# Kernel tuning notes

Hardware: AMD Instinct MI355X
Metric: run time of the kernel (lower is better)

## Reference

```python
import jax, jax.numpy as jnp
import numpy as np

LMAX = 3
D_IRREP = (LMAX + 1) ** 2  # 16
EPS = 1e-5


def _conv1d(x, w, pad):
    # x: [N, C_in, L], w: [C_out, C_in, K] -> [N, C_out, L]
    return jax.lax.conv_general_dilated(
        x, w, window_strides=(1,), padding=[(pad, pad)],
        dimension_numbers=("NCH", "OIH", "NCH"))


def setup_inputs() -> dict:
    key = jax.random.key(0)
    ks = jax.random.split(key, 8)
    B, Cin, Cout, N, K, RES = 128, 256, 256, 64, 5, 8
    return {
        "x": jax.random.normal(ks[0], (B, Cin * D_IRREP, N), jnp.float32),
        "weight": jax.random.normal(ks[1], (LMAX + 1, Cout, Cin, K), jnp.float32) / np.sqrt(Cin * K).astype(np.float32),
        "bias": jax.random.normal(ks[2], (1, 1, Cout), jnp.float32) * 0.02,
        "affine_weight": jnp.ones((LMAX + 1, Cout), jnp.float32),
        "gating_w": jax.random.normal(ks[3], (Cout, Cout), jnp.float32) / np.sqrt(Cout).astype(np.float32),
        "gating_b": jnp.zeros((Cout,), jnp.float32),
        "to_grid": jax.random.normal(ks[4], (RES, RES, D_IRREP), jnp.float32) * 0.3,
        "from_grid": jax.random.normal(ks[5], (RES, RES, D_IRREP), jnp.float32) * 0.3,
    }


def reference(x, weight, bias, affine_weight, gating_w, gating_b, to_grid, from_grid):
    B, CI, N = x.shape
    Cin = CI // D_IRREP
    Cout = weight.shape[1]
    pad = weight.shape[-1] // 2
    x = x.reshape(B, Cin, D_IRREP, N)

    # per-degree Conv1d over the time axis, irrep order folded into batch
    h_parts = []
    for l in range(LMAX + 1):
        lo, li = l * l, 2 * l + 1
        x_l = x[:, :, lo:lo + li, :]                                  # [B, Cin, li, N]
        x_l = x_l.transpose(0, 2, 1, 3).reshape(B * li, Cin, N)       # (b i) c n
        h_l = _conv1d(x_l, weight[l], pad)                            # [B*li, Cout, N]
        h_l = h_l.reshape(B, li, Cout, N).transpose(0, 3, 1, 2).reshape(B * N, li, Cout)  # (b n) i c
        if l == 0:
            h_l = h_l + bias
        h_parts.append(h_l)
    h = jnp.concatenate(h_parts, axis=1)                              # [B*N, 16, Cout]

    # rms_norm_sh: center l=0 over channels, degree-balanced RMS, per-degree affine
    degrees = np.repeat(np.arange(LMAX + 1), 2 * np.arange(LMAX + 1) + 1)  # [16]
    bal = jnp.asarray((1.0 / (2.0 * degrees + 1.0)) / (LMAX + 1), h.dtype)  # [16]
    mean0 = jnp.mean(h[:, :1, :], axis=2, keepdims=True)
    h = jnp.concatenate([h[:, :1, :] - mean0, h[:, 1:, :]], axis=1)
    var = jnp.einsum("zic,i->zc", h * h, bal)                         # [Z, C]
    inv = jax.lax.rsqrt(jnp.mean(var, axis=-1)[:, None, None] + EPS)  # [Z,1,1]
    h = h * inv * affine_weight[degrees][None]                        # [Z,16,C]

    # SeparableS2Activation: SiLU-gated scalars + S2 grid activation for l>0
    gate = jax.nn.silu(h[:, :1, :] @ gating_w.T + gating_b)           # [Z,1,C]
    grid = jax.nn.silu(jnp.einsum("bai,zic->zbac", to_grid, h))       # [Z,8,8,C]
    s2 = jnp.einsum("bai,zbac->zic", from_grid, grid)                 # [Z,16,C]
    h = jnp.concatenate([gate, s2[:, 1:, :]], axis=1)

    # (b n) i c -> b (c i) n
    out = h.reshape(B, N, D_IRREP, Cout).transpose(0, 3, 2, 1).reshape(B, Cout * D_IRREP, N)
    return out
```

## Files before the change

kernel.cpp:

```cpp
#include <hip/hip_runtime.h>
#include <hip/hip_bf16.h>

#define BB    128
#define CIN   256
#define COUT  256
#define NN    64
#define KW    5
#define DIRR  16
#define ZTOT  (BB*NN)
#define SX    264

typedef __attribute__((ext_vector_type(4))) float f32x4;
typedef __attribute__((ext_vector_type(8))) short s16x8;

__device__ inline ushort f2bf(float f) {
    __hip_bfloat16 h = __float2bfloat16(f);
    return *(const ushort*)&h;
}
__device__ inline float bf2f(ushort u) {
    union { unsigned int ui; float f; } cv; cv.ui = ((unsigned int)u) << 16;
    return cv.f;
}
__device__ inline void gload_lds16(const void* g, void* l) {
    __builtin_amdgcn_global_load_lds(
        (const __attribute__((address_space(1))) void*)g,
        (__attribute__((address_space(3))) void*)l, 16, 0, 0);
}
__device__ inline float wave_sum(float v) {
    #pragma unroll
    for (int o = 32; o > 0; o >>= 1) v += __shfl_down(v, o, 64);
    return v;
}
__device__ inline float silu(float x) { return x / (1.f + __expf(-x)); }

__global__ __launch_bounds__(256) void pack_w_k(const float* __restrict__ w,
                                                ushort* __restrict__ wb)
{
    int idx = blockIdx.x * 256 + threadIdx.x;
    int cl = idx & 31;
    int c  = (idx >> 5) & 255;
    int ch = (idx >> 13) & 7;
    int k  = (idx >> 16) % 5;
    int l  = idx / 327680;
    int cin = ch * 32 + cl;
    wb[idx] = f2bf(w[(((size_t)(l * COUT + c) * CIN) + cin) * KW + k]);
}

__global__ __launch_bounds__(256) void pack2_k(const float* __restrict__ gw,
                                               const float* __restrict__ tg,
                                               const float* __restrict__ fg,
                                               ushort* __restrict__ gwb,
                                               ushort* __restrict__ tgb,
                                               ushort* __restrict__ fgTb)
{
    int idx = blockIdx.x * 256 + threadIdx.x;
    if (idx < 65536) {
        gwb[idx] = f2bf(gw[idx]);
    } else if (idx < 66560) {
        int j = idx - 65536;
        tgb[j] = f2bf(tg[j]);
    } else if (idx < 67584) {
        int j = idx - 66560;
        int p = j >> 4, i = j & 15;
        fgTb[i * 64 + p] = f2bf(fg[j]);
    }
}

__global__ __launch_bounds__(256) void conv_mfma_k(const float* __restrict__ x,
                                                   const ushort* __restrict__ wb,
                                                   const float* __restrict__ bias,
                                                   ushort* __restrict__ hbuf)
{
    __shared__ __align__(16) ushort xs[68 * SX];
    __shared__ __align__(16) ushort bs[2][COUT * 32];

    const int tid  = threadIdx.x;
    const int lane = tid & 63;
    const int wid  = tid >> 6;
    const int blk  = blockIdx.x;
    const int b = blk >> 4, i = blk & 15;
    const int l = (i == 0) ? 0 : (i < 4) ? 1 : (i < 9) ? 2 : 3;

    {
        const float4* xb = (const float4*)(x + (((size_t)b * CIN) * DIRR + i) * NN);
        #pragma unroll
        for (int p = 0; p < 16; ++p) {
            int idx = p * 256 + tid;
            int cin = idx >> 4, f4 = idx & 15;
            float4 v = xb[(size_t)cin * (DIRR * NN / 4) + f4];
            ushort* dst = xs + (size_t)(2 + f4 * 4) * SX + cin;
            dst[0]      = f2bf(v.x);
            dst[SX]     = f2bf(v.y);
            dst[2 * SX] = f2bf(v.z);
            dst[3 * SX] = f2bf(v.w);
        }
        xs[ 0 * SX + tid] = 0; xs[ 1 * SX + tid] = 0;
        xs[66 * SX + tid] = 0; xs[67 * SX + tid] = 0;
    }

    const ushort* wl = wb + (size_t)l * (5 * 8 * COUT * 32);
    auto stageB = [&](int s, int ch, int buf) {
        const char* src = (const char*)(wl + (size_t)(s * 8 + ch) * COUT * 32);
        char* dst = (char*)bs[buf];
        #pragma unroll
        for (int q = 0; q < 4; ++q) {
            int d = q * 4096 + tid * 16;
            gload_lds16(src + d, dst + d);
        }
    };

    stageB(0, 0, 0);
    __syncthreads();

    f32x4 acc[4][4];
    #pragma unroll
    for (int m = 0; m < 4; ++m)
        #pragma unroll
        for (int j = 0; j < 4; ++j) acc[m][j] = (f32x4){0.f, 0.f, 0.f, 0.f};

    const int kb = lane >> 4;
    const int lr = lane & 15;

    int step = 0;
    #pragma unroll 1
    for (int s = 0; s < 5; ++s) {
        #pragma unroll 1
        for (int ch = 0; ch < 8; ++ch, ++step) {
            int cur = step & 1;
            int ns  = (ch == 7) ? s + 1 : s;
            int nch = (ch == 7) ? 0 : ch + 1;
            if (ns < 5) stageB(ns, nch, cur ^ 1);

            int cin0 = ch * 32;
            s16x8 av[4], bv[4];
            #pragma unroll
            for (int m = 0; m < 4; ++m) {
                int r = m * 16 + lr + s;
                av[m] = *(const s16x8*)(xs + (size_t)r * SX + cin0 + kb * 8);
            }
            #pragma unroll
            for (int j = 0; j < 4; ++j) {
                int c = wid * 64 + j * 16 + lr;
                bv[j] = *(const s16x8*)(bs[cur] + (size_t)c * 32 + kb * 8);
            }
            #pragma unroll
            for (int m = 0; m < 4; ++m)
                #pragma unroll
                for (int j = 0; j < 4; ++j)
                    acc[m][j] = __builtin_amdgcn_mfma_f32_16x16x32_bf16(av[m], bv[j], acc[m][j], 0, 0, 0);
            __syncthreads();
        }
    }

    const int row0 = (lane >> 4) * 4;
    #pragma unroll
    for (int j = 0; j < 4; ++j) {
        int c = wid * 64 + j * 16 + lr;
        float bvv = (i == 0) ? bias[c] : 0.f;
        #pragma unroll
        for (int m = 0; m < 4; ++m)
            #pragma unroll
            for (int r = 0; r < 4; ++r) {
                int n = m * 16 + row0 + r;
                size_t z = (size_t)b * NN + n;
                hbuf[(z * DIRR + i) * COUT + c] = f2bf(acc[m][j][r] + bvv);
            }
    }
}

__global__ __launch_bounds__(256) void norm_k(const ushort* __restrict__ hbuf,
                                              const float* __restrict__ afw,
                                              ushort* __restrict__ hn2,
                                              ushort* __restrict__ hn0)
{
    __shared__ float red[8];
    const int z0 = blockIdx.x * 2;
    const int c = threadIdx.x;
    const int lane = c & 63, w = c >> 6;

    float hv[2][16];
    #pragma unroll
    for (int zz = 0; zz < 2; ++zz)
        #pragma unroll
        for (int i = 0; i < 16; ++i)
            hv[zz][i] = bf2f(hbuf[((size_t)(z0 + zz) * DIRR + i) * COUT + c]);

    float s0 = wave_sum(hv[0][0]);
    float s1 = wave_sum(hv[1][0]);
    if (lane == 0) { red[w] = s0; red[4 + w] = s1; }
    __syncthreads();
    float m0 = (red[0] + red[1] + red[2] + red[3]) * (1.f / 256.f);
    float m1 = (red[4] + red[5] + red[6] + red[7]) * (1.f / 256.f);
    hv[0][0] -= m0;
    hv[1][0] -= m1;

    const float bal[4] = {0.25f, 1.f / 12.f, 1.f / 20.f, 1.f / 28.f};
    float var[2];
    #pragma unroll
    for (int zz = 0; zz < 2; ++zz) {
        float v = bal[0] * hv[zz][0] * hv[zz][0];
        #pragma unroll
        for (int i = 1; i < 16; ++i) {
            int li = (i < 4) ? 1 : (i < 9) ? 2 : 3;
            v += bal[li] * hv[zz][i] * hv[zz][i];
        }
        var[zz] = v;
    }
    float v0 = wave_sum(var[0]);
    float v1 = wave_sum(var[1]);
    __syncthreads();
    if (lane == 0) { red[w] = v0; red[4 + w] = v1; }
    __syncthreads();
    float inv[2];
    inv[0] = rsqrtf((red[0] + red[1] + red[2] + red[3]) * (1.f / 256.f) + 1e-5f);
    inv[1] = rsqrtf((red[4] + red[5] + red[6] + red[7]) * (1.f / 256.f) + 1e-5f);

    float a0 = afw[c], a1 = afw[COUT + c], a2 = afw[2 * COUT + c], a3 = afw[3 * COUT + c];
    #pragma unroll
    for (int zz = 0; zz < 2; ++zz) {
        s16x8 o0, o1;
        #pragma unroll
        for (int i = 0; i < 16; ++i) {
            float al = (i == 0) ? a0 : (i < 4) ? a1 : (i < 9) ? a2 : a3;
            ushort ub = f2bf(hv[zz][i] * inv[zz] * al);
            if (i < 8) o0[i] = (short)ub; else o1[i - 8] = (short)ub;
        }
        ushort* dst = hn2 + ((size_t)c * ZTOT + z0 + zz) * DIRR;
        *(s16x8*)dst = o0;
        *(s16x8*)(dst + 8) = o1;
        hn0[(size_t)(z0 + zz) * COUT + c] = (ushort)(unsigned short)o0[0];
    }
}

__global__ __launch_bounds__(256) void gate_k(const ushort* __restrict__ hn0,
                                              const ushort* __restrict__ gwb,
                                              const float* __restrict__ gb,
                                              float* __restrict__ out)
{
    const int b = blockIdx.x;
    const int tid = threadIdx.x;
    const int lane = tid & 63, w = tid >> 6;
    const int lr = lane & 15, kb = lane >> 4;

    f32x4 acc[4][4];
    #pragma unroll
    for (int m = 0; m < 4; ++m)
        #pragma unroll
        for (int n = 0; n < 4; ++n) acc[m][n] = (f32x4){0.f, 0.f, 0.f, 0.f};

    #pragma unroll 1
    for (int ks = 0; ks < 8; ++ks) {
        s16x8 av[4], bv[4];
        #pragma unroll
        for (int m = 0; m < 4; ++m)
            av[m] = *(const s16x8*)(hn0 + ((size_t)(b * 64 + m * 16 + lr) * 256 + ks * 32 + kb * 8));
        #pragma unroll
        for (int n = 0; n < 4; ++n)
            bv[n] = *(const s16x8*)(gwb + ((size_t)(w * 64 + n * 16 + lr) * 256 + ks * 32 + kb * 8));
        #pragma unroll
        for (int m = 0; m < 4; ++m)
            #pragma unroll
            for (int n = 0; n < 4; ++n)
                acc[m][n] = __builtin_amdgcn_mfma_f32_16x16x32_bf16(av[m], bv[n], acc[m][n], 0, 0, 0);
    }

    #pragma unroll
    for (int n = 0; n < 4; ++n) {
        int c = w * 64 + n * 16 + lr;
        float gbc = gb[c];
        #pragma unroll
        for (int m = 0; m < 4; ++m)
            #pragma unroll
            for (int r = 0; r < 4; ++r) {
                int nrow = m * 16 + kb * 4 + r;
                out[((size_t)b * COUT + c) * (DIRR * NN) + nrow] = silu(acc[m][n][r] + gbc);
            }
    }
}

__global__ __launch_bounds__(256) void grid_k(const ushort* __restrict__ hn2,
                                              const ushort* __restrict__ tgb,
                                              const ushort* __restrict__ fgTb,
                                              float* __restrict__ out)
{
    __shared__ __align__(16) char lds[36864 + 2048 + 2304];
    ushort* P_s  = (ushort*)lds;
    float*  S_s  = (float*)lds;
    ushort* tg_s = (ushort*)(lds + 36864);
    ushort* fgT_s= (ushort*)(lds + 36864 + 2048);

    const int bid = blockIdx.x;
    const int c  = bid & 255;
    const int zt = bid >> 8;
    const int z0 = zt * 256;
    const int tid = threadIdx.x;
    const int lane = tid & 63, w = tid >> 6;
    const int lr = lane & 15, kb = lane >> 4;

    #pragma unroll
    for (int q = 0; q < 4; ++q) {
        int idx = q * 256 + tid;
        tg_s[idx] = tgb[idx];
        int i = idx >> 6, p = idx & 63;
        fgT_s[i * 72 + p] = fgTb[idx];
    }
    __syncthreads();

    f32x4 acc[4][4];
    #pragma unroll
    for (int m = 0; m < 4; ++m)
        #pragma unroll
        for (int n = 0; n < 4; ++n) acc[m][n] = (f32x4){0.f, 0.f, 0.f, 0.f};

    s16x8 bv[4];
    #pragma unroll
    for (int n = 0; n < 4; ++n)
        bv[n] = (kb < 2) ? *(const s16x8*)(tg_s + (n * 16 + lr) * 16 + kb * 8)
                         : (s16x8){0,0,0,0,0,0,0,0};
    #pragma unroll
    for (int m = 0; m < 4; ++m) {
        int zl = w * 64 + m * 16 + lr;
        s16x8 av = (kb < 2) ? *(const s16x8*)(hn2 + ((size_t)c * ZTOT + z0 + zl) * DIRR + kb * 8)
                            : (s16x8){0,0,0,0,0,0,0,0};
        #pragma unroll
        for (int n = 0; n < 4; ++n)
            acc[m][n] = __builtin_amdgcn_mfma_f32_16x16x32_bf16(av, bv[n], acc[m][n], 0, 0, 0);
    }

    #pragma unroll
    for (int m = 0; m < 4; ++m)
        #pragma unroll
        for (int n = 0; n < 4; ++n)
            #pragma unroll
            for (int r = 0; r < 4; ++r) {
                int zl = w * 64 + m * 16 + kb * 4 + r;
                int p  = n * 16 + lr;
                P_s[zl * 72 + p] = f2bf(silu(acc[m][n][r]));
            }

    f32x4 acc2[4];
    #pragma unroll
    for (int m = 0; m < 4; ++m) acc2[m] = (f32x4){0.f, 0.f, 0.f, 0.f};
    #pragma unroll
    for (int ks = 0; ks < 2; ++ks) {
        s16x8 bv2 = *(const s16x8*)(fgT_s + lr * 72 + ks * 32 + kb * 8);
        #pragma unroll
        for (int m = 0; m < 4; ++m) {
            s16x8 av2 = *(const s16x8*)(P_s + (w * 64 + m * 16 + lr) * 72 + ks * 32 + kb * 8);
            acc2[m] = __builtin_amdgcn_mfma_f32_16x16x32_bf16(av2, bv2, acc2[m], 0, 0, 0);
        }
    }

    __syncthreads();

    #pragma unroll
    for (int m = 0; m < 4; ++m)
        #pragma unroll
        for (int r = 0; r < 4; ++r) {
            int zl = w * 64 + m * 16 + kb * 4 + r;
            S_s[zl * 17 + lr] = acc2[m][r];
        }
    __syncthreads();

    const int bb = tid >> 6, n = tid & 63;
    const int b0 = zt * 4;
    const float* srow = S_s + (bb * 64 + n) * 17;
    float* obase = out + ((size_t)(b0 + bb) * COUT + c) * (DIRR * NN) + n;
    #pragma unroll
    for (int i = 1; i < 16; ++i)
        obase[i * NN] = srow[i];
}

__global__ __launch_bounds__(256) void post_k(const ushort* __restrict__ hbuf,
                                              const float* __restrict__ afw,
                                              const float* __restrict__ gw,
                                              const float* __restrict__ gb,
                                              const float* __restrict__ tg,
                                              const float* __restrict__ fg,
                                              float* __restrict__ out)
{
    __shared__ float h0s[COUT];
    __shared__ float red[4];
    __shared__ float tgs[64 * 16];
    __shared__ float fgs[64 * 16];

    int z = blockIdx.x;
    int c = threadIdx.x;
    int b = z >> 6, n = z & 63;
    int lane = c & 63, wid = c >> 6;

    for (int idx = c; idx < 1024; idx += 256) { tgs[idx] = tg[idx]; fgs[idx] = fg[idx]; }

    float hv[16];
    #pragma unroll
    for (int i = 0; i < 16; ++i)
        hv[i] = bf2f(hbuf[((size_t)z * DIRR + i) * COUT + c]);

    float s0 = wave_sum(hv[0]);
    if (lane == 0) red[wid] = s0;
    __syncthreads();
    float mean0 = (red[0] + red[1] + red[2] + red[3]) * (1.f / 256.f);
    hv[0] -= mean0;

    const float bal[4] = {0.25f, 1.f / 12.f, 1.f / 20.f, 1.f / 28.f};
    float var = bal[0] * hv[0] * hv[0];
    #pragma unroll
    for (int i = 1; i < 16; ++i) {
        int li = (i < 4) ? 1 : (i < 9) ? 2 : 3;
        var += bal[li] * hv[i] * hv[i];
    }
    float s1 = wave_sum(var);
    __syncthreads();
    if (lane == 0) red[wid] = s1;
    __syncthreads();
    float inv = rsqrtf((red[0] + red[1] + red[2] + red[3]) * (1.f / 256.f) + 1e-5f);

    float a0 = afw[c], a1 = afw[COUT + c], a2 = afw[2 * COUT + c], a3 = afw[3 * COUT + c];
    #pragma unroll
    for (int i = 0; i < 16; ++i) {
        float al = (i == 0) ? a0 : (i < 4) ? a1 : (i < 9) ? a2 : a3;
        hv[i] *= inv * al;
    }
    h0s[c] = hv[0];
    __syncthreads();

    float g = gb[c];
    const float4* gwr = (const float4*)(gw + (size_t)c * COUT);
    #pragma unroll 4
    for (int j = 0; j < 64; ++j) {
        float4 wv = gwr[j];
        g += h0s[4 * j] * wv.x + h0s[4 * j + 1] * wv.y + h0s[4 * j + 2] * wv.z + h0s[4 * j + 3] * wv.w;
    }
    float gate = silu(g);

    float s2a[16];
    #pragma unroll
    for (int i = 0; i < 16; ++i) s2a[i] = 0.f;
    #pragma unroll 1
    for (int p = 0; p < 64; ++p) {
        float gv = 0.f;
        #pragma unroll
        for (int i = 0; i < 16; ++i) gv += tgs[p * 16 + i] * hv[i];
        gv = silu(gv);
        #pragma unroll
        for (int i = 0; i < 16; ++i) s2a[i] += fgs[p * 16 + i] * gv;
    }

    float* ob = out + (size_t)b * COUT * DIRR * NN + (size_t)c * DIRR * NN + n;
    ob[0] = gate;
    #pragma unroll
    for (int i = 1; i < 16; ++i) ob[i * NN] = s2a[i];
}

extern "C" void kernel_launch(void* const* d_in, const int* in_sizes, int n_in,
                              void* d_out, int out_size, void* d_ws, size_t ws_size,
                              hipStream_t stream)
{
    const float* x    = (const float*)d_in[0];
    const float* w    = (const float*)d_in[1];
    const float* bias = (const float*)d_in[2];
    const float* afw  = (const float*)d_in[3];
    const float* gw   = (const float*)d_in[4];
    const float* gb   = (const float*)d_in[5];
    const float* tg   = (const float*)d_in[6];
    const float* fg   = (const float*)d_in[7];
    float* out = (float*)d_out;

    const size_t off_hbuf = 0;
    const size_t off_wb   = 67108864;
    const size_t off_hn2  = 69730304;
    const size_t off_hn0  = off_hn2 + 67108864;
    const size_t off_gwb  = off_hn0 + 4194304;
    const size_t off_tgb  = off_gwb + 131072;
    const size_t off_fgT  = off_tgb + 2048;
    const size_t need     = off_fgT + 2048;

    ushort* hbuf = (ushort*)((char*)d_ws + off_hbuf);
    ushort* wb   = (ushort*)((char*)d_ws + off_wb);

    pack_w_k   <<<5120, 256, 0, stream>>>(w, wb);
    conv_mfma_k<<<BB * DIRR, 256, 0, stream>>>(x, wb, bias, hbuf);

    if (ws_size >= need) {
        ushort* hn2  = (ushort*)((char*)d_ws + off_hn2);
        ushort* hn0  = (ushort*)((char*)d_ws + off_hn0);
        ushort* gwb  = (ushort*)((char*)d_ws + off_gwb);
        ushort* tgb  = (ushort*)((char*)d_ws + off_tgb);
        ushort* fgTb = (ushort*)((char*)d_ws + off_fgT);

        pack2_k<<<264, 256, 0, stream>>>(gw, tg, fg, gwb, tgb, fgTb);
        norm_k <<<ZTOT / 2, 256, 0, stream>>>(hbuf, afw, hn2, hn0);
        gate_k <<<BB, 256, 0, stream>>>(hn0, gwb, gb, out);
        grid_k <<<256 * (ZTOT / 256), 256, 0, stream>>>(hn2, tgb, fgTb, out);
    } else {
        post_k<<<ZTOT, 256, 0, stream>>>(hbuf, afw, gw, gb, tg, fg, out);
    }
}
```

Baseline: 276.0 us.

## Load conv weights directly from global memory, drop LDS double-buffering and barriers

Weight fragments for the conv MFMA loop are now read straight from global memory (served through L2/L1) into registers, replacing the double-buffered LDS staging via global_load_lds and the per-step __syncthreads. The x tile load is also re-indexed so consecutive threads write consecutive cin entries in LDS. The aim is to remove barrier stalls and LDS traffic and to free LDS for higher occupancy. The cost is that every wave issues its own global loads with no explicit prefetch, so latency is exposed unless the unroll and occupancy hide it.

```diff
diff --git a/kernel.cpp b/kernel.cpp
--- a/kernel.cpp
+++ b/kernel.cpp
@@ -20,11 +20,6 @@
 __device__ inline float bf2f(ushort u) {
     union { unsigned int ui; float f; } cv; cv.ui = ((unsigned int)u) << 16;
     return cv.f;
-}
-__device__ inline void gload_lds16(const void* g, void* l) {
-    __builtin_amdgcn_global_load_lds(
-        (const __attribute__((address_space(1))) void*)g,
-        (__attribute__((address_space(3))) void*)l, 16, 0, 0);
 }
 __device__ inline float wave_sum(float v) {
     #pragma unroll
@@ -72,7 +67,6 @@
                                                    ushort* __restrict__ hbuf)
 {
     __shared__ __align__(16) ushort xs[68 * SX];
-    __shared__ __align__(16) ushort bs[2][COUT * 32];
 
     const int tid  = threadIdx.x;
     const int lane = tid & 63;
@@ -85,10 +79,10 @@
         const float4* xb = (const float4*)(x + (((size_t)b * CIN) * DIRR + i) * NN);
         #pragma unroll
         for (int p = 0; p < 16; ++p) {
-            int idx = p * 256 + tid;
-            int cin = idx >> 4, f4 = idx & 15;
-            float4 v = xb[(size_t)cin * (DIRR * NN / 4) + f4];
-            ushort* dst = xs + (size_t)(2 + f4 * 4) * SX + cin;
+            int cin = (tid & 63) | ((p & 3) << 6);
+            int nq  = ((tid >> 6) << 2) | (p >> 2);
+            float4 v = xb[(size_t)cin * (DIRR * NN / 4) + nq];
+            ushort* dst = xs + (size_t)(2 + nq * 4) * SX + cin;
             dst[0]      = f2bf(v.x);
             dst[SX]     = f2bf(v.y);
             dst[2 * SX] = f2bf(v.z);
@@ -97,19 +91,6 @@
         xs[ 0 * SX + tid] = 0; xs[ 1 * SX + tid] = 0;
         xs[66 * SX + tid] = 0; xs[67 * SX + tid] = 0;
     }
-
-    const ushort* wl = wb + (size_t)l * (5 * 8 * COUT * 32);
-    auto stageB = [&](int s, int ch, int buf) {
-        const char* src = (const char*)(wl + (size_t)(s * 8 + ch) * COUT * 32);
-        char* dst = (char*)bs[buf];
-        #pragma unroll
-        for (int q = 0; q < 4; ++q) {
-            int d = q * 4096 + tid * 16;
-            gload_lds16(src + d, dst + d);
-        }
-    };
-
-    stageB(0, 0, 0);
     __syncthreads();
 
     f32x4 acc[4][4];
@@ -121,34 +102,40 @@
     const int kb = lane >> 4;
     const int lr = lane & 15;
 
-    int step = 0;
+    const ushort* wl = wb + (size_t)l * (5 * 8 * 8192);
+    int boffB[4];
+    #pragma unroll
+    for (int j = 0; j < 4; ++j)
+        boffB[j] = (wid * 64 + j * 16 + lr) * 32 + kb * 8;
+
+    const ushort* arow[4];
+    #pragma unroll
+    for (int m = 0; m < 4; ++m)
+        arow[m] = xs + (size_t)(m * 16 + lr) * SX + kb * 8;
+
     #pragma unroll 1
     for (int s = 0; s < 5; ++s) {
-        #pragma unroll 1
-        for (int ch = 0; ch < 8; ++ch, ++step) {
-            int cur = step & 1;
-            int ns  = (ch == 7) ? s + 1 : s;
-            int nch = (ch == 7) ? 0 : ch + 1;
-            if (ns < 5) stageB(ns, nch, cur ^ 1);
-
-            int cin0 = ch * 32;
-            s16x8 av[4], bv[4];
-            #pragma unroll
-            for (int m = 0; m < 4; ++m) {
-                int r = m * 16 + lr + s;
-                av[m] = *(const s16x8*)(xs + (size_t)r * SX + cin0 + kb * 8);
-            }
-            #pragma unroll
-            for (int j = 0; j < 4; ++j) {
-                int c = wid * 64 + j * 16 + lr;
-                bv[j] = *(const s16x8*)(bs[cur] + (size_t)c * 32 + kb * 8);
-            }
+        const ushort* bt_s = wl + (size_t)s * 8 * 8192;
+        const ushort* ar_s0 = arow[0] + s * SX;
+        const ushort* ar_s1 = arow[1] + s * SX;
+        const ushort* ar_s2 = arow[2] + s * SX;
+        const ushort* ar_s3 = arow[3] + s * SX;
+        #pragma unroll 2
+        for (int ch = 0; ch < 8; ++ch) {
+            const ushort* bt = bt_s + ch * 8192;
+            s16x8 bv[4], av[4];
+            #pragma unroll
+            for (int j = 0; j < 4; ++j)
+                bv[j] = *(const s16x8*)(bt + boffB[j]);
+            av[0] = *(const s16x8*)(ar_s0 + ch * 32);
+            av[1] = *(const s16x8*)(ar_s1 + ch * 32);
+            av[2] = *(const s16x8*)(ar_s2 + ch * 32);
+            av[3] = *(const s16x8*)(ar_s3 + ch * 32);
             #pragma unroll
             for (int m = 0; m < 4; ++m)
                 #pragma unroll
                 for (int j = 0; j < 4; ++j)
                     acc[m][j] = __builtin_amdgcn_mfma_f32_16x16x32_bf16(av[m], bv[j], acc[m][j], 0, 0, 0);
-            __syncthreads();
         }
     }
 
```

New measurement: 255.6 us. 1.08x faster.
